# Optimization experiments

Hardware: AMD Instinct MI355X
Metric: run time of the kernel (lower is better)

The kernel has to match this reference:

```python
import jax, jax.numpy as jnp
import numpy as np

N = 16384       # nodes (hits in one event)
IN_DIM = 9      # input features per hit
HID = 128       # hidden_dim
PROP = 64       # propagate_dimensions; 2*PROP == HID so all gravnet layers share shapes
SPACE = 4       # learned space dimensions
K = 40          # neighbors (includes self, matching torch_cluster.knn)
L = 4           # num_gravnet_layers
OUT_DIM = 4


def _lin(key, fan_in, fan_out):
    # torch nn.Linear default init: U(-1/sqrt(fan_in), 1/sqrt(fan_in))
    k1, k2 = jax.random.split(key)
    lim = 1.0 / np.sqrt(fan_in)
    W = jax.random.uniform(k1, (fan_in, fan_out), minval=-lim, maxval=lim, dtype=jnp.float32)
    b = jax.random.uniform(k2, (fan_out,), minval=-lim, maxval=lim, dtype=jnp.float32)
    return W, b


def _stack_lin(key, fan_in, fan_out, n):
    Ws, bs = [], []
    for i in range(n):
        W, b = _lin(jax.random.fold_in(key, i), fan_in, fan_out)
        Ws.append(W); bs.append(b)
    return jnp.stack(Ws), jnp.stack(bs)


def setup_inputs() -> dict:
    key = jax.random.key(0)
    ks = jax.random.split(key, 16)
    inp = {}
    inp['x'] = jax.random.normal(ks[0], (N, IN_DIM), dtype=jnp.float32)
    inp['fc1_W'], inp['fc1_b'] = _lin(ks[1], IN_DIM, HID)
    inp['fc2_W'], inp['fc2_b'] = _lin(ks[2], HID, HID)
    # GravNetConv params (in_channels = HID = 2*PROP for every layer)
    inp['gs_W'], inp['gs_b'] = _stack_lin(ks[3], HID, SPACE, L)          # lin_s
    inp['gh_W'], inp['gh_b'] = _stack_lin(ks[4], HID, PROP, L)           # lin_h
    inp['go_W'], inp['go_b'] = _stack_lin(ks[5], HID + 2 * PROP, 2 * PROP, L)  # lin_out
    # dense_after_gravnet: Linear(2P->HID), Linear(HID->HID), Linear(HID->2P)
    inp['d1_W'], inp['d1_b'] = _stack_lin(ks[6], 2 * PROP, HID, L)
    inp['d2_W'], inp['d2_b'] = _stack_lin(ks[7], HID, HID, L)
    inp['d3_W'], inp['d3_b'] = _stack_lin(ks[8], HID, 2 * PROP, L)
    inp['fc3_W'], inp['fc3_b'] = _lin(ks[9], 2 * PROP, HID)
    inp['fc4_W'], inp['fc4_b'] = _lin(ks[10], HID, OUT_DIM)
    return inp


def _gravnet_layer(x, sW, sb, hW, hb, oW, ob):
    # PyG GravNetConv: s = lin_s(x), h = lin_h(x); kNN in s-space (self included);
    # edge weight exp(-10*d^2); message h_j*w; aggr = [mean, max]; out = lin_out([x, aggr]).
    s = x @ sW + sb                               # [N, SPACE]
    h = x @ hW + hb                               # [N, PROP]
    s2 = jnp.sum(s * s, axis=1)
    d2 = s2[:, None] + s2[None, :] - 2.0 * (s @ s.T)   # [N, N] squared distances
    neg_d2, idx = jax.lax.top_k(-d2, K)           # k nearest (self is its own nearest)
    w = jnp.exp(10.0 * jnp.minimum(neg_d2, 0.0))  # exp(-10*d2), clamped d2 >= 0
    msg = h[idx] * w[..., None]                   # [N, K, PROP] gather + weight
    agg = jnp.concatenate([msg.mean(axis=1), msg.max(axis=1)], axis=-1)  # [N, 2P]
    return jnp.concatenate([x, agg], axis=-1) @ oW + ob


def reference(x, fc1_W, fc1_b, fc2_W, fc2_b, gs_W, gs_b, gh_W, gh_b, go_W, go_b,
              d1_W, d1_b, d2_W, d2_b, d3_W, d3_b, fc3_W, fc3_b, fc4_W, fc4_b):
    relu = jax.nn.relu
    x = relu(x @ fc1_W + fc1_b)
    x = relu(x @ fc2_W + fc2_b)
    for i in range(L):  # small fixed layer count
        x = _gravnet_layer(x, gs_W[i], gs_b[i], gh_W[i], gh_b[i], go_W[i], go_b[i])
        x = relu(x @ d1_W[i] + d1_b[i])
        x = relu(x @ d2_W[i] + d2_b[i])
        x = relu(x @ d3_W[i] + d3_b[i])
    x = relu(x @ fc3_W + fc3_b)
    return x @ fc4_W + fc4_b
```

## Files before the change

kernel.cpp:

```cpp
#include <hip/hip_runtime.h>
#include <math.h>

#define NPTS     16384
#define KNN_K    40
#define KNN_CAPW 320

typedef unsigned short u16;
typedef __attribute__((ext_vector_type(8))) short bf16x8;
typedef __attribute__((ext_vector_type(4))) float f32x4;

static __device__ __forceinline__ float bf2f(unsigned short h) {
  return __uint_as_float(((unsigned)h) << 16);
}
static __device__ __forceinline__ unsigned short f2bf(float f) {
  unsigned u = __float_as_uint(f);
  unsigned r = (u + 0x7fffu + ((u >> 16) & 1u)) >> 16;
  return (unsigned short)r;
}
static __device__ __forceinline__ float ldf(const float* p) { return *p; }
static __device__ __forceinline__ float ldf(const unsigned short* p) { return bf2f(*p); }

static __device__ __forceinline__ float rfl(float x) {
  return __uint_as_float(__builtin_amdgcn_readfirstlane(__float_as_uint(x)));
}
static __device__ __forceinline__ unsigned mbcnt64(unsigned long long m) {
  return __builtin_amdgcn_mbcnt_hi((unsigned)(m >> 32),
                                   __builtin_amdgcn_mbcnt_lo((unsigned)m, 0u));
}

static __device__ __forceinline__ unsigned encf(float f) {
  unsigned b = __float_as_uint(f);
  return (b & 0x80000000u) ? ~b : (b | 0x80000000u);
}
static __device__ __forceinline__ float decf(unsigned e) {
  unsigned b = (e & 0x80000000u) ? (e ^ 0x80000000u) : ~e;
  return __uint_as_float(b);
}

#define WSPLIT_ELEMS 393216

__global__ __launch_bounds__(256, 8) void wsplit_k(
    const float* __restrict__ fc2W, const float* __restrict__ ghW,
    const float* __restrict__ goW,  const float* __restrict__ d1W,
    const float* __restrict__ d2W,  const float* __restrict__ d3W,
    const float* __restrict__ fc3W, u16* __restrict__ out)
{
  int e = blockIdx.x * 256 + threadIdx.x;
  const float* W; int base, M, K;
  if (e < 16384)       { W = fc2W; base = 0;      M = 128; K = 128; }
  else if (e < 49152)  { W = ghW;  base = 16384;  M = 64;  K = 128; }
  else if (e < 180224) { W = goW;  base = 49152;  M = 128; K = 256; }
  else if (e < 245760) { W = d1W;  base = 180224; M = 128; K = 128; }
  else if (e < 311296) { W = d2W;  base = 245760; M = 128; K = 128; }
  else if (e < 376832) { W = d3W;  base = 311296; M = 128; K = 128; }
  else                 { W = fc3W; base = 376832; M = 128; K = 128; }
  int li = e - base;
  float wv = W[li];
  u16 hi = f2bf(wv);
  u16 lo = f2bf(wv - bf2f(hi));
  int row = li / M;
  int n   = li % M;
  int l   = row / K;
  int kl  = row % K;
  int p   = n >> 6, c = n & 63;
  int kb  = kl >> 5, kk = kl & 31;
  u16* ob = out + 2 * base + l * (2 * K * M) + p * (K * 128) + kb * 4096;
  ob[c * 32 + kk] = hi;
  ob[2048 + c * 32 + kk] = lo;
}

template<bool RELU>
__global__ __launch_bounds__(256, 2) void gemm_mfma_k(
    const u16* __restrict__ A1, int lda1,
    const u16* __restrict__ A2, int lda2, int K1,
    const u16* __restrict__ Wsp, int pstride, const float* __restrict__ bias,
    u16* __restrict__ C, int ldc, int K)
{
  constexpr int MCOLS = 64;
  constexpr int AST = 40;
  __shared__ u16 lds[64 * AST + 2 * MCOLS * AST];
  u16* As = lds;
  u16* Wh = lds + 64 * AST;
  u16* Wl = Wh + MCOLS * AST;

  const int tid = threadIdx.x;
  const int lane = tid & 63;
  const int w = tid >> 6;
  const int panel = blockIdx.x >> 8;
  const int row0 = (blockIdx.x & 255) * 64;
  Wsp += (size_t)panel * pstride;
  bias += panel * 64;
  C += panel * 64;

  f32x4 acc[4];
  #pragma unroll
  for (int rt = 0; rt < 4; ++rt)
    acc[rt] = (f32x4){0.f, 0.f, 0.f, 0.f};

  const int rbase = lane & 15;
  const int koff = (lane >> 4) * 8;

  for (int k0 = 0, kb = 0; k0 < K; k0 += 32, ++kb) {
    __syncthreads();
    {
      int r = tid >> 2, seg = tid & 3;
      int kk = k0 + seg * 8;
      const u16* src = (kk < K1) ? &A1[(size_t)(row0 + r) * lda1 + kk]
                                 : &A2[(size_t)(row0 + r) * lda2 + (kk - K1)];
      *(uint4*)&As[r * AST + seg * 8] = *(const uint4*)src;
    }
    {
      const u16* wsb = Wsp + (size_t)kb * 4096;
      #pragma unroll
      for (int l = tid; l < 2 * MCOLS * 4; l += 256) {
        int r = l >> 2, seg = l & 3;
        *(uint4*)&Wh[r * AST + seg * 8] = *(const uint4*)&wsb[r * 32 + seg * 8];
      }
    }
    __syncthreads();

    bf16x8 a[4];
    #pragma unroll
    for (int rt = 0; rt < 4; ++rt)
      a[rt] = *(const bf16x8*)&As[(rt * 16 + rbase) * AST + koff];
    {
      int col = w * 16 + rbase;
      bf16x8 bh = *(const bf16x8*)&Wh[col * AST + koff];
      bf16x8 bl = *(const bf16x8*)&Wl[col * AST + koff];
      #pragma unroll
      for (int rt = 0; rt < 4; ++rt) {
        acc[rt] = __builtin_amdgcn_mfma_f32_16x16x32_bf16(a[rt], bh, acc[rt], 0, 0, 0);
        acc[rt] = __builtin_amdgcn_mfma_f32_16x16x32_bf16(a[rt], bl, acc[rt], 0, 0, 0);
      }
    }
  }

  __syncthreads();
  constexpr int CST = MCOLS + 8;
  u16* Ct = lds;
  const int rq = (lane >> 4) * 4;
  {
    int col = w * 16 + rbase;
    float bv = bias[col];
    #pragma unroll
    for (int rt = 0; rt < 4; ++rt) {
      #pragma unroll
      for (int q = 0; q < 4; ++q) {
        float v = acc[rt][q] + bv;
        if (RELU) v = fmaxf(v, 0.f);
        Ct[(rt * 16 + rq + q) * CST + col] = f2bf(v);
      }
    }
  }
  __syncthreads();
  constexpr int SEGS = MCOLS / 8;
  for (int l = tid; l < 64 * SEGS; l += 256) {
    int r = l / SEGS, sg = l % SEGS;
    *(uint4*)&C[(size_t)(row0 + r) * ldc + sg * 8] = *(const uint4*)&Ct[r * CST + sg * 8];
  }
}

template<int MCOLS, bool RELU>
__global__ __launch_bounds__(256, 2) void gemm_mfma_f32_k(
    const u16* __restrict__ A1, int lda1,
    const u16* __restrict__ A2, int lda2, int K1,
    const float* __restrict__ W, const float* __restrict__ bias,
    u16* __restrict__ C, int ldc, int K)
{
  constexpr int CT = MCOLS / 64;
  constexpr int AST = 40;
  __shared__ u16 lds[64 * AST + 2 * MCOLS * AST];
  u16* As = lds;
  u16* Wh = lds + 64 * AST;
  u16* Wl = Wh + MCOLS * AST;

  const int tid = threadIdx.x;
  const int lane = tid & 63;
  const int w = tid >> 6;
  const int row0 = blockIdx.x * 64;

  f32x4 acc[4][CT];
  #pragma unroll
  for (int rt = 0; rt < 4; ++rt)
    #pragma unroll
    for (int ct = 0; ct < CT; ++ct)
      acc[rt][ct] = (f32x4){0.f, 0.f, 0.f, 0.f};

  const int rbase = lane & 15;
  const int koff = (lane >> 4) * 8;

  for (int k0 = 0; k0 < K; k0 += 32) {
    __syncthreads();
    {
      int r = tid >> 2, seg = tid & 3;
      int kk = k0 + seg * 8;
      const u16* src = (kk < K1) ? &A1[(size_t)(row0 + r) * lda1 + kk]
                                 : &A2[(size_t)(row0 + r) * lda2 + (kk - K1)];
      *(uint4*)&As[r * AST + seg * 8] = *(const uint4*)src;
    }
    for (int l = tid; l < 32 * MCOLS; l += 256) {
      int n = l & (MCOLS - 1), kk = l / MCOLS;
      float wv = W[(size_t)(k0 + kk) * MCOLS + n];
      u16 h = f2bf(wv);
      Wh[n * AST + kk] = h;
      Wl[n * AST + kk] = f2bf(wv - bf2f(h));
    }
    __syncthreads();

    bf16x8 a[4];
    #pragma unroll
    for (int rt = 0; rt < 4; ++rt)
      a[rt] = *(const bf16x8*)&As[(rt * 16 + rbase) * AST + koff];
    #pragma unroll
    for (int ct = 0; ct < CT; ++ct) {
      int col = (w * CT + ct) * 16 + rbase;
      bf16x8 bh = *(const bf16x8*)&Wh[col * AST + koff];
      bf16x8 bl = *(const bf16x8*)&Wl[col * AST + koff];
      #pragma unroll
      for (int rt = 0; rt < 4; ++rt) {
        acc[rt][ct] = __builtin_amdgcn_mfma_f32_16x16x32_bf16(a[rt], bh, acc[rt][ct], 0, 0, 0);
        acc[rt][ct] = __builtin_amdgcn_mfma_f32_16x16x32_bf16(a[rt], bl, acc[rt][ct], 0, 0, 0);
      }
    }
  }

  __syncthreads();
  constexpr int CST = MCOLS + 8;
  u16* Ct = lds;
  const int rq = (lane >> 4) * 4;
  #pragma unroll
  for (int ct = 0; ct < CT; ++ct) {
    int col = (w * CT + ct) * 16 + rbase;
    float bv = bias[col];
    #pragma unroll
    for (int rt = 0; rt < 4; ++rt) {
      #pragma unroll
      for (int q = 0; q < 4; ++q) {
        float v = acc[rt][ct][q] + bv;
        if (RELU) v = fmaxf(v, 0.f);
        Ct[(rt * 16 + rq + q) * CST + col] = f2bf(v);
      }
    }
  }
  __syncthreads();
  constexpr int SEGS = MCOLS / 8;
  for (int l = tid; l < 64 * SEGS; l += 256) {
    int r = l / SEGS, sg = l % SEGS;
    *(uint4*)&C[(size_t)(row0 + r) * ldc + sg * 8] = *(const uint4*)&Ct[r * CST + sg * 8];
  }
}

template<int MCOLS, bool RELU, typename TIN, typename TOUT>
__global__ __launch_bounds__(256, 4) void gemm_k(
    const TIN* __restrict__ A1, int lda1,
    const TIN* __restrict__ A2, int lda2, int K1,
    const float* __restrict__ W, const float* __restrict__ bias,
    TOUT* __restrict__ C, int ldc, int K)
{
  constexpr int TCS = MCOLS / 8;
  constexpr int RPT = (64 * TCS) / 256;
  __shared__ float Asl[64][33];
  __shared__ float Ws[32][MCOLS];
  const int tid = threadIdx.x;
  const int row0 = blockIdx.x * 64;
  const int tc = tid % TCS, tr = tid / TCS;

  float acc[RPT][8];
  #pragma unroll
  for (int p = 0; p < RPT; ++p)
    #pragma unroll
    for (int q = 0; q < 8; ++q) acc[p][q] = 0.f;

  for (int k0 = 0; k0 < K; k0 += 32) {
    __syncthreads();
    for (int l = tid; l < 64 * 32; l += 256) {
      int r = l >> 5, c = l & 31, k = k0 + c;
      float v = 0.f;
      if (k < K) v = (k < K1) ? ldf(&A1[(size_t)(row0 + r) * lda1 + k])
                              : ldf(&A2[(size_t)(row0 + r) * lda2 + (k - K1)]);
      Asl[r][c] = v;
    }
    for (int l = tid; l < 32 * MCOLS; l += 256) {
      int kr = l / MCOLS, c = l % MCOLS, k = k0 + kr;
      Ws[kr][c] = (k < K) ? W[(size_t)k * MCOLS + c] : 0.f;
    }
    __syncthreads();
    #pragma unroll
    for (int kk = 0; kk < 32; ++kk) {
      float a[RPT];
      #pragma unroll
      for (int p = 0; p < RPT; ++p) a[p] = Asl[tr * RPT + p][kk];
      const float4 w0 = *(const float4*)&Ws[kk][tc * 8];
      const float4 w1 = *(const float4*)&Ws[kk][tc * 8 + 4];
      #pragma unroll
      for (int p = 0; p < RPT; ++p) {
        acc[p][0] = fmaf(a[p], w0.x, acc[p][0]);
        acc[p][1] = fmaf(a[p], w0.y, acc[p][1]);
        acc[p][2] = fmaf(a[p], w0.z, acc[p][2]);
        acc[p][3] = fmaf(a[p], w0.w, acc[p][3]);
        acc[p][4] = fmaf(a[p], w1.x, acc[p][4]);
        acc[p][5] = fmaf(a[p], w1.y, acc[p][5]);
        acc[p][6] = fmaf(a[p], w1.z, acc[p][6]);
        acc[p][7] = fmaf(a[p], w1.w, acc[p][7]);
      }
    }
  }

  const float4 b0 = *(const float4*)&bias[tc * 8];
  const float4 b1 = *(const float4*)&bias[tc * 8 + 4];
  #pragma unroll
  for (int p = 0; p < RPT; ++p) {
    int r = row0 + tr * RPT + p;
    float o[8];
    o[0] = acc[p][0] + b0.x; o[1] = acc[p][1] + b0.y;
    o[2] = acc[p][2] + b0.z; o[3] = acc[p][3] + b0.w;
    o[4] = acc[p][4] + b1.x; o[5] = acc[p][5] + b1.y;
    o[6] = acc[p][6] + b1.z; o[7] = acc[p][7] + b1.w;
    if (RELU) {
      #pragma unroll
      for (int q = 0; q < 8; ++q) o[q] = fmaxf(o[q], 0.f);
    }
    if constexpr (sizeof(TOUT) == 2) {
      unsigned p0 = (unsigned)f2bf(o[0]) | ((unsigned)f2bf(o[1]) << 16);
      unsigned p1 = (unsigned)f2bf(o[2]) | ((unsigned)f2bf(o[3]) << 16);
      unsigned p2 = (unsigned)f2bf(o[4]) | ((unsigned)f2bf(o[5]) << 16);
      unsigned p3 = (unsigned)f2bf(o[6]) | ((unsigned)f2bf(o[7]) << 16);
      uint4 pk = make_uint4(p0, p1, p2, p3);
      *(uint4*)&C[(size_t)r * ldc + tc * 8] = pk;
    } else {
      float4 o0, o1;
      o0.x = o[0]; o0.y = o[1]; o0.z = o[2]; o0.w = o[3];
      o1.x = o[4]; o1.y = o[5]; o1.z = o[6]; o1.w = o[7];
      *(float4*)&C[(size_t)r * ldc + tc * 8] = o0;
      *(float4*)&C[(size_t)r * ldc + tc * 8 + 4] = o1;
    }
  }
}

template<bool RELU, bool MM, typename TOUT>
__global__ __launch_bounds__(256, 4) void gemm4_k(
    const u16* __restrict__ A, int lda,
    const float* __restrict__ W, const float* __restrict__ bias,
    TOUT* __restrict__ C, int K, unsigned* mm)
{
  __shared__ float Wsl[128 * 4];
  __shared__ float bl[4];
  const int tid = threadIdx.x;
  for (int l = tid; l < K * 4; l += 256) Wsl[l] = W[l];
  if (tid < 4) bl[tid] = bias[tid];
  __syncthreads();
  const int row = blockIdx.x * 256 + tid;
  const u16* ap = A + (size_t)row * lda;
  float a0 = bl[0], a1 = bl[1], a2 = bl[2], a3 = bl[3];
  for (int k8 = 0; k8 < K; k8 += 8) {
    uint4 pk = *(const uint4*)&ap[k8];
    unsigned uu[4] = {pk.x, pk.y, pk.z, pk.w};
    #pragma unroll
    for (int q = 0; q < 4; ++q) {
      float flo = __uint_as_float(uu[q] << 16);
      float fhi = __uint_as_float(uu[q] & 0xFFFF0000u);
      const float* wr0 = &Wsl[(k8 + 2 * q) * 4];
      a0 = fmaf(flo, wr0[0], a0); a1 = fmaf(flo, wr0[1], a1);
      a2 = fmaf(flo, wr0[2], a2); a3 = fmaf(flo, wr0[3], a3);
      a0 = fmaf(fhi, wr0[4], a0); a1 = fmaf(fhi, wr0[5], a1);
      a2 = fmaf(fhi, wr0[6], a2); a3 = fmaf(fhi, wr0[7], a3);
    }
  }
  if (RELU) {
    a0 = fmaxf(a0, 0.f); a1 = fmaxf(a1, 0.f);
    a2 = fmaxf(a2, 0.f); a3 = fmaxf(a3, 0.f);
  }
  if constexpr (sizeof(TOUT) == 2) {
    C[(size_t)row * 4 + 0] = (TOUT)f2bf(a0);
    C[(size_t)row * 4 + 1] = (TOUT)f2bf(a1);
    C[(size_t)row * 4 + 2] = (TOUT)f2bf(a2);
    C[(size_t)row * 4 + 3] = (TOUT)f2bf(a3);
  } else {
    float4 o; o.x = a0; o.y = a1; o.z = a2; o.w = a3;
    *(float4*)&C[(size_t)row * 4] = o;
  }
  if constexpr (MM) {
    float mn0 = a0, mx0 = a0, mn1 = a1, mx1 = a1;
    float mn2 = a2, mx2 = a2, mn3 = a3, mx3 = a3;
    #pragma unroll
    for (int o = 32; o >= 1; o >>= 1) {
      mn0 = fminf(mn0, __shfl_xor(mn0, o, 64)); mx0 = fmaxf(mx0, __shfl_xor(mx0, o, 64));
      mn1 = fminf(mn1, __shfl_xor(mn1, o, 64)); mx1 = fmaxf(mx1, __shfl_xor(mx1, o, 64));
      mn2 = fminf(mn2, __shfl_xor(mn2, o, 64)); mx2 = fmaxf(mx2, __shfl_xor(mx2, o, 64));
      mn3 = fminf(mn3, __shfl_xor(mn3, o, 64)); mx3 = fmaxf(mx3, __shfl_xor(mx3, o, 64));
    }
    if ((tid & 63) == 0) {
      atomicMin(&mm[0], encf(mn0)); atomicMax(&mm[4], encf(mx0));
      atomicMin(&mm[1], encf(mn1)); atomicMax(&mm[5], encf(mx1));
      atomicMin(&mm[2], encf(mn2)); atomicMax(&mm[6], encf(mx2));
      atomicMin(&mm[3], encf(mn3)); atomicMax(&mm[7], encf(mx3));
    }
  }
}

__global__ void init_mm_k(unsigned* mm) {
  int t = threadIdx.x;
  if (t < 4) { mm[t] = 0xFFFFFFFFu; mm[4 + t] = 0u; }
}

static __device__ __forceinline__ float dimsel(float4 p, int d) {
  return (d == 0) ? p.x : (d == 1) ? p.y : (d == 2) ? p.z : p.w;
}

__global__ __launch_bounds__(1024, 1) void histpref_k(
    const float* __restrict__ S, unsigned* __restrict__ mm,
    unsigned* __restrict__ binoff)
{
  __shared__ unsigned hist[256];
  __shared__ unsigned wsum[4];
  const int tid = threadIdx.x;
  float mn[4], rg[4];
  #pragma unroll
  for (int d = 0; d < 4; ++d) {
    mn[d] = decf(mm[d]);
    rg[d] = decf(mm[4 + d]) - mn[d];
  }
  int a = 0;
  #pragma unroll
  for (int d = 1; d < 4; ++d) if (rg[d] > rg[a]) a = d;
  int b = (a == 0) ? 1 : 0;
  #pragma unroll
  for (int d = 0; d < 4; ++d) if (d != a && rg[d] > rg[b]) b = d;
  float inva = (rg[a] > 0.f) ? (16.f / rg[a]) * 0.999999f : 0.f;
  float invb = (rg[b] > 0.f) ? (16.f / rg[b]) * 0.999999f : 0.f;
  if (tid == 0) {
    mm[8] = (unsigned)a; mm[9] = (unsigned)b;
    mm[10] = __float_as_uint(mn[a]); mm[11] = __float_as_uint(inva);
    mm[12] = __float_as_uint(mn[b]); mm[13] = __float_as_uint(invb);
  }
  if (tid < 256) hist[tid] = 0u;
  __syncthreads();
  for (int i = tid; i < NPTS; i += 1024) {
    float4 p = *(const float4*)&S[(size_t)i * 4];
    int ba = min(15, max(0, (int)((dimsel(p, a) - mn[a]) * inva)));
    int bb = min(15, max(0, (int)((dimsel(p, b) - mn[b]) * invb)));
    atomicAdd(&hist[ba * 16 + bb], 1u);
  }
  __syncthreads();
  unsigned v = 0, x = 0;
  if (tid < 256) {
    int lane = tid & 63;
    v = hist[tid]; x = v;
    #pragma unroll
    for (int o = 1; o < 64; o <<= 1) {
      unsigned t = (unsigned)__shfl_up((int)x, o, 64);
      if (lane >= o) x += t;
    }
    if (lane == 63) wsum[tid >> 6] = x;
  }
  __syncthreads();
  if (tid < 256) {
    unsigned off = 0;
    for (int k = 0; k < (tid >> 6); ++k) off += wsum[k];
    binoff[tid] = off + x - v;
  }
}

__global__ __launch_bounds__(256, 4) void scatter_k(
    const float* __restrict__ S, const unsigned* __restrict__ mm,
    unsigned* __restrict__ binoff,
    float4* __restrict__ SX4, float* __restrict__ SS2, u16* __restrict__ SIDXs)
{
  int a = (int)mm[8], b = (int)mm[9];
  float alo = __uint_as_float(mm[10]), inva = __uint_as_float(mm[11]);
  float blo = __uint_as_float(mm[12]), invb = __uint_as_float(mm[13]);
  int i = blockIdx.x * 256 + threadIdx.x;
  float4 p = *(const float4*)&S[(size_t)i * 4];
  int ba = min(15, max(0, (int)((dimsel(p, a) - alo) * inva)));
  int bb = min(15, max(0, (int)((dimsel(p, b) - blo) * invb)));
  unsigned pos = atomicAdd(&binoff[ba * 16 + bb], 1u);
  SX4[pos] = p;
  SS2[pos] = fmaf(p.x, p.x, fmaf(p.y, p.y, fmaf(p.z, p.z, p.w * p.w)));
  SIDXs[pos] = (u16)i;
}

__global__ __launch_bounds__(512, 4) void gaabb_k(const float4* __restrict__ SX4,
                                                  float* __restrict__ gaabb) {
  int w = threadIdx.x >> 6, lane = threadIdx.x & 63;
  int g = blockIdx.x * 8 + w;
  float4 p = SX4[g * 64 + lane];
  float mnx = p.x, mny = p.y, mnz = p.z, mnw = p.w;
  float mxx = p.x, mxy = p.y, mxz = p.z, mxw = p.w;
  #pragma unroll
  for (int o = 32; o >= 1; o >>= 1) {
    mnx = fminf(mnx, __shfl_xor(mnx, o, 64)); mxx = fmaxf(mxx, __shfl_xor(mxx, o, 64));
    mny = fminf(mny, __shfl_xor(mny, o, 64)); mxy = fmaxf(mxy, __shfl_xor(mxy, o, 64));
    mnz = fminf(mnz, __shfl_xor(mnz, o, 64)); mxz = fmaxf(mxz, __shfl_xor(mxz, o, 64));
    mnw = fminf(mnw, __shfl_xor(mnw, o, 64)); mxw = fmaxf(mxw, __shfl_xor(mxw, o, 64));
  }
  if (lane == 0) {
    float4* gp = (float4*)&gaabb[g * 8];
    gp[0] = make_float4(mnx, mny, mnz, mnw);
    gp[1] = make_float4(mxx, mxy, mxz, mxw);
  }
}

struct CompactRes { int cnt; unsigned thr; };

static __device__ __forceinline__ CompactRes compact_buf(unsigned* bufR, int cnt, int lane) {
  int n = min(cnt, KNN_CAPW);
  int lo = -1, hi = 0x7FFFFFFF, chi = n;
  for (int it = 0; it < 32; ++it) {
    if (chi <= 96) break;
    int mid = lo + ((hi - lo) >> 1);
    int lc = 0;
    for (int base = 0; base < n; base += 64) {
      int i = base + lane;
      bool c = (i < n) && (bufR[i] <= (unsigned)mid);
      lc += (int)__popcll(__ballot(c));
    }
    if (lc >= 40) { hi = mid; chi = lc; } else lo = mid;
  }
  unsigned thr = (unsigned)hi;
  int out = 0;
  for (int base = 0; base < n; base += 64) {
    int i = base + lane;
    unsigned key = (i < n) ? bufR[i] : 0xFFFFFFFFu;
    bool keep = (i < n) && (key <= thr);
    unsigned long long mk = __ballot(keep);
    unsigned pre = mbcnt64(mk);
    if (keep) bufR[out + (int)pre] = key;
    out += (int)__popcll(mk);
  }
  CompactRes r; r.cnt = out; r.thr = thr;
  return r;
}

__global__ __launch_bounds__(256, 4) void knn_k(
    const float4* __restrict__ SX4, const float* __restrict__ SS2,
    const u16* __restrict__ SIDXs, const float* __restrict__ gaabb,
    u16* __restrict__ idx_out, u16* __restrict__ w_out)
{
  __shared__ unsigned buf[4 * 4 * KNN_CAPW];
  __shared__ unsigned scr[4 * 128];
  __shared__ int cnts[16];
  __shared__ unsigned thrend[16];
  __shared__ unsigned short glist[4 * 64];
  __shared__ unsigned long long mws[4];
  __shared__ unsigned thrsh[4];

  const int tid = threadIdx.x;
  const int lane = tid & 63;
  const int w = tid >> 6;
  const int sp0 = blockIdx.x * 4;

  float cx[4], cy[4], cz[4], cw[4], s2r[4], thrF[4];
  int orow[4], cnt[4];
  #pragma unroll
  for (int r = 0; r < 4; ++r) {
    float4 sr = SX4[sp0 + r];
    cx[r] = rfl(-2.f * sr.x); cy[r] = rfl(-2.f * sr.y);
    cz[r] = rfl(-2.f * sr.z); cw[r] = rfl(-2.f * sr.w);
    s2r[r] = rfl(fmaf(sr.x, sr.x, fmaf(sr.y, sr.y, fmaf(sr.z, sr.z, sr.w * sr.w))));
    orow[r] = SIDXs[sp0 + r];
    cnt[r] = 0;
  }
  unsigned* bufw = &buf[w * 4 * KNN_CAPW];
  unsigned* mph = buf;

  {
    int gs = sp0 >> 6;
    int g0 = min(max(gs - 7, 0), 240);
    float m1[4], m2[4];
    #pragma unroll
    for (int r = 0; r < 4; ++r) { m1[r] = 3.0e38f; m2[r] = 3.0e38f; }
    #pragma unroll
    for (int gi = 0; gi < 4; ++gi) {
      int j = (g0 + w * 4 + gi) * 64 + lane;
      float4 p = SX4[j];
      float q = SS2[j];
      #pragma unroll
      for (int r = 0; r < 4; ++r) {
        float d = fmaf(cx[r], p.x, fmaf(cy[r], p.y, fmaf(cz[r], p.z,
                  fmaf(cw[r], p.w, q + s2r[r]))));
        d = fmaxf(d, 0.f);
        bool lt1 = d < m1[r];
        float nm2 = lt1 ? m1[r] : fminf(m2[r], d);
        m1[r] = fminf(m1[r], d);
        m2[r] = nm2;
      }
    }
    #pragma unroll
    for (int r = 0; r < 4; ++r) {
      mph[(r * 8 + w * 2 + 0) * 64 + lane] = __float_as_uint(m1[r]);
      mph[(r * 8 + w * 2 + 1) * 64 + lane] = __float_as_uint(m2[r]);
    }
  }
  __syncthreads();

  {
    unsigned m1 = 0xFFFFFFFFu, m2 = 0xFFFFFFFFu;
    #pragma unroll
    for (int s = 0; s < 8; ++s) {
      unsigned v = mph[(w * 8 + s) * 64 + lane];
      bool lt = v < m1;
      unsigned nm2 = lt ? m1 : min(m2, v);
      m1 = min(m1, v);
      m2 = nm2;
    }
    unsigned e0 = m1, e1 = m2;
    #pragma unroll
    for (int k = 2; k <= 128; k <<= 1) {
      #pragma unroll
      for (int jj = k >> 1; jj >= 1; jj >>= 1) {
        bool up = (((lane * 2) & k) == 0);
        if (jj == 1) {
          unsigned a = min(e0, e1), b = max(e0, e1);
          e0 = up ? a : b; e1 = up ? b : a;
        } else {
          int lj = jj >> 1;
          bool lower = ((lane & lj) == 0);
          bool tm = (up == lower);
          unsigned o0 = (unsigned)__shfl_xor((int)e0, lj, 64);
          e0 = tm ? min(e0, o0) : max(e0, o0);
          unsigned o1 = (unsigned)__shfl_xor((int)e1, lj, 64);
          e1 = tm ? min(e1, o1) : max(e1, o1);
        }
      }
    }
    unsigned v40 = (unsigned)__shfl((int)e1, 19, 64);
    if (lane == 0) thrsh[w] = v40;
  }
  __syncthreads();
  #pragma unroll
  for (int r = 0; r < 4; ++r) thrF[r] = __uint_as_float(thrsh[r]);

  {
    int g = w * 64 + lane;
    float4 mn = *(const float4*)&gaabb[g * 8];
    float4 mx = *(const float4*)&gaabb[g * 8 + 4];
    bool want = false;
    #pragma unroll
    for (int r = 0; r < 4; ++r) {
      float px = -0.5f * cx[r], py = -0.5f * cy[r];
      float pz = -0.5f * cz[r], pw = -0.5f * cw[r];
      float dx = fmaxf(fmaxf(mn.x - px, px - mx.x), 0.f);
      float dy = fmaxf(fmaxf(mn.y - py, py - mx.y), 0.f);
      float dz = fmaxf(fmaxf(mn.z - pz, pz - mx.z), 0.f);
      float dw = fmaxf(fmaxf(mn.w - pw, pw - mx.w), 0.f);
      float md = fmaf(dx, dx, fmaf(dy, dy, fmaf(dz, dz, dw * dw)));
      want |= (md <= thrF[r]);
    }
    unsigned long long bal = __ballot(want);
    if (lane == 0) mws[w] = bal;
  }
  __syncthreads();

  int ng = 0;
  {
    int ordbase = 0;
    #pragma unroll
    for (int pgi = 0; pgi < 4; ++pgi) {
      unsigned long long m = mws[pgi];
      bool want = (m >> lane) & 1ull;
      int ord = ordbase + (int)mbcnt64(m);
      if (want && ((ord & 3) == w))
        glist[w * 64 + (ord >> 2)] = (unsigned short)(pgi * 64 + lane);
      ordbase += (int)__popcll(m);
    }
    ng = (ordbase + 3 - w) >> 2;
  }

  if (ng > 0) {
    int j = (int)glist[w * 64] * 64 + lane;
    float4 p = SX4[j];
    float q = SS2[j];
    unsigned sv = (unsigned)j;
    for (int i = 0; i < ng; ++i) {
      float4 pn = p; float qn = q; unsigned svn = sv;
      if (i + 1 < ng) {
        int j2 = (int)glist[w * 64 + i + 1] * 64 + lane;
        pn = SX4[j2]; qn = SS2[j2]; svn = (unsigned)j2;
      }
      #pragma unroll
      for (int r = 0; r < 4; ++r) {
        float d = fmaf(cx[r], p.x, fmaf(cy[r], p.y, fmaf(cz[r], p.z,
                  fmaf(cw[r], p.w, q + s2r[r]))));
        bool k = d <= thrF[r];
        unsigned long long mk = __ballot(k);
        if (mk) {
          int pos = cnt[r] + (int)mbcnt64(mk);
          if (k) bufw[r * KNN_CAPW + pos] =
              (__float_as_uint(fmaxf(d, 0.f)) & 0xFFFFC000u) | sv;
          cnt[r] += (int)__popcll(mk);
          if (cnt[r] >= KNN_CAPW - 64) {
            CompactRes cr = compact_buf(&bufw[r * KNN_CAPW], cnt[r], lane);
            cnt[r] = cr.cnt;
            thrF[r] = __uint_as_float((cr.thr & 0xFFFFC000u) | 0x3FFFu);
          }
        }
      }
      p = pn; q = qn; sv = svn;
    }
  }

  if (lane == 0) {
    #pragma unroll
    for (int r = 0; r < 4; ++r) {
      cnts[w * 4 + r] = cnt[r];
      thrend[w * 4 + r] = (__float_as_uint(thrF[r]) & 0xFFFFC000u) | 0x3FFFu;
    }
  }
  __syncthreads();

  {
    const int rr = w;
    const unsigned* seg[4];
    int c[4], off[5];
    off[0] = 0;
    #pragma unroll
    for (int s = 0; s < 4; ++s) {
      seg[s] = &buf[(s * 4 + rr) * KNN_CAPW];
      c[s] = cnts[s * 4 + rr];
      off[s + 1] = off[s] + c[s];
    }
    int mt = off[4];
    unsigned* S = &scr[rr * 128];

    if (mt > 128) {
      unsigned hi0 = min(min(thrend[0 * 4 + rr], thrend[1 * 4 + rr]),
                         min(thrend[2 * 4 + rr], thrend[3 * 4 + rr]));
      int lc = 0;
      #pragma unroll
      for (int s = 0; s < 4; ++s)
        for (int base = 0; base < c[s]; base += 64) {
          int i = base + lane;
          bool cc = (i < c[s]) && (seg[s][i] <= hi0);
          lc += (int)__popcll(__ballot(cc));
        }
      unsigned thrm = hi0;
      if (lc > 128) {
        int lo = -1, hi = (int)hi0, chi = lc;
        for (int it = 0; it < 32; ++it) {
          if (chi <= 96) break;
          int mid = lo + ((hi - lo) >> 1);
          int lc2 = 0;
          #pragma unroll
          for (int s = 0; s < 4; ++s)
            for (int base = 0; base < c[s]; base += 64) {
              int i = base + lane;
              bool cc = (i < c[s]) && (seg[s][i] <= (unsigned)mid);
              lc2 += (int)__popcll(__ballot(cc));
            }
          if (lc2 >= 40) { hi = mid; chi = lc2; } else lo = mid;
        }
        thrm = (unsigned)hi;
      }
      int out = 0;
      #pragma unroll
      for (int s = 0; s < 4; ++s)
        for (int base = 0; base < c[s]; base += 64) {
          int i = base + lane;
          unsigned key = (i < c[s]) ? seg[s][i] : 0xFFFFFFFFu;
          bool keep = (i < c[s]) && (key <= thrm);
          unsigned long long mk = __ballot(keep);
          int pos = out + (int)mbcnt64(mk);
          if (keep && pos < 128) S[pos] = key;
          out += (int)__popcll(mk);
        }
      mt = min(out, 128);
    } else {
      #pragma unroll
      for (int s = 0; s < 4; ++s)
        for (int base = 0; base < c[s]; base += 64) {
          int i = base + lane;
          if (i < c[s]) S[off[s] + i] = seg[s][i];
        }
    }

    const float fx = cx[rr], fy = cy[rr], fz = cz[rr], fw = cw[rr];
    const float s2i = s2r[rr];
    const int row = orow[rr];

    unsigned long long e0 = ~0ull, e1 = ~0ull;
    {
      int sl0 = lane * 2, sl1 = lane * 2 + 1;
      if (sl0 < mt) {
        unsigned key = S[sl0];
        unsigned sj = key & 0x3FFFu;
        float4 p = SX4[sj];
        float qj = fmaf(p.x, p.x, fmaf(p.y, p.y, fmaf(p.z, p.z, p.w * p.w)));
        float d = fmaf(fx, p.x, fmaf(fy, p.y, fmaf(fz, p.z, fmaf(fw, p.w, qj + s2i))));
        unsigned oi = (unsigned)SIDXs[sj];
        e0 = (((unsigned long long)__float_as_uint(fmaxf(d, 0.f))) << 32) | oi;
      }
      if (sl1 < mt) {
        unsigned key = S[sl1];
        unsigned sj = key & 0x3FFFu;
        float4 p = SX4[sj];
        float qj = fmaf(p.x, p.x, fmaf(p.y, p.y, fmaf(p.z, p.z, p.w * p.w)));
        float d = fmaf(fx, p.x, fmaf(fy, p.y, fmaf(fz, p.z, fmaf(fw, p.w, qj + s2i))));
        unsigned oi = (unsigned)SIDXs[sj];
        e1 = (((unsigned long long)__float_as_uint(fmaxf(d, 0.f))) << 32) | oi;
      }
    }

    #pragma unroll
    for (int k = 2; k <= 128; k <<= 1) {
      #pragma unroll
      for (int jj = k >> 1; jj >= 1; jj >>= 1) {
        bool up = (((lane * 2) & k) == 0);
        if (jj == 1) {
          unsigned long long a = (e0 < e1) ? e0 : e1;
          unsigned long long b = (e0 < e1) ? e1 : e0;
          e0 = up ? a : b; e1 = up ? b : a;
        } else {
          int lj = jj >> 1;
          bool lower = ((lane & lj) == 0);
          bool tm = (up == lower);
          unsigned long long o0 = __shfl_xor(e0, lj, 64);
          e0 = tm ? ((e0 < o0) ? e0 : o0) : ((e0 > o0) ? e0 : o0);
          unsigned long long o1 = __shfl_xor(e1, lj, 64);
          e1 = tm ? ((e1 < o1) ? e1 : o1) : ((e1 > o1) ? e1 : o1);
        }
      }
    }

    const int ob = row * KNN_K;
    if (lane < 20) {
      int v0 = lane * 2;
      idx_out[ob + v0] = (unsigned short)(e0 & 0xFFFFu);
      w_out[ob + v0] = f2bf(__expf(-10.f * __uint_as_float((unsigned)(e0 >> 32))));
      int v1 = v0 + 1;
      idx_out[ob + v1] = (unsigned short)(e1 & 0xFFFFu);
      w_out[ob + v1] = f2bf(__expf(-10.f * __uint_as_float((unsigned)(e1 >> 32))));
    }
  }
}

__global__ __launch_bounds__(256, 4) void agg_k(
    const unsigned short* __restrict__ h, const unsigned short* __restrict__ idxb,
    const unsigned short* __restrict__ wb, unsigned short* __restrict__ Aout)
{
  const int row = blockIdx.x * 4 + (threadIdx.x >> 6);
  const int lane = threadIdx.x & 63;
  const int base = row * KNN_K;
  float mean = 0.f, mx = -INFINITY;
  #pragma unroll 4
  for (int k = 0; k < KNN_K; ++k) {
    int j = idxb[base + k];
    float wv = bf2f(wb[base + k]);
    float m = bf2f(h[(size_t)j * 64 + lane]) * wv;
    mean += m;
    mx = fmaxf(mx, m);
  }
  Aout[(size_t)row * 128 + lane] = f2bf(mean * (1.f / 40.f));
  Aout[(size_t)row * 128 + 64 + lane] = f2bf(mx);
}

extern "C" void kernel_launch(void* const* d_in, const int* in_sizes, int n_in,
                              void* d_out, int out_size, void* d_ws, size_t ws_size,
                              hipStream_t stream)
{
  const float* x    = (const float*)d_in[0];
  const float* fc1W = (const float*)d_in[1];  const float* fc1b = (const float*)d_in[2];
  const float* fc2W = (const float*)d_in[3];  const float* fc2b = (const float*)d_in[4];
  const float* gsW  = (const float*)d_in[5];  const float* gsb  = (const float*)d_in[6];
  const float* ghW  = (const float*)d_in[7];  const float* ghb  = (const float*)d_in[8];
  const float* goW  = (const float*)d_in[9];  const float* gob  = (const float*)d_in[10];
  const float* d1W  = (const float*)d_in[11]; const float* d1b  = (const float*)d_in[12];
  const float* d2W  = (const float*)d_in[13]; const float* d2b  = (const float*)d_in[14];
  const float* d3W  = (const float*)d_in[15]; const float* d3b  = (const float*)d_in[16];
  const float* fc3W = (const float*)d_in[17]; const float* fc3b = (const float*)d_in[18];
  const float* fc4W = (const float*)d_in[19]; const float* fc4b = (const float*)d_in[20];
  float* out = (float*)d_out;

  const size_t N = NPTS;
  u16* X    = (u16*)d_ws;
  u16* Abuf = X + N * 128;
  u16* T    = Abuf + N * 128;
  u16* IDX  = T + N * 128;
  u16* WNB  = IDX + N * 40;
  float4* SX4g = (float4*)(WNB + N * 40);
  float*  SS2g = (float*)(SX4g + N);
  u16*    SIDXg = (u16*)(SS2g + N);
  unsigned* binoff = (unsigned*)(SIDXg + N);
  unsigned* mm     = binoff + 256;
  float* gaabbg    = (float*)(mm + 16);
  float* S = (float*)Abuf;
  u16* H = T;

  u16* WSPL = (u16*)(gaabbg + 256 * 8);
  size_t needed = (size_t)((char*)(WSPL + 2ull * WSPLIT_ELEMS) - (char*)d_ws);
  const bool PRE = ws_size >= needed;

  const size_t OF_FC2 = 0,      OF_GH = 32768, OF_GO = 98304;
  const size_t OF_D1 = 360448,  OF_D2 = 491520, OF_D3 = 622592, OF_FC3 = 753664;
  const int PS_128 = 16384;
  const int PS_256 = 32768;
  const size_t LS_GH = 16384, LS_GO = 65536, LS_D = 32768;

  if (PRE) {
    wsplit_k<<<WSPLIT_ELEMS / 256, 256, 0, stream>>>(
        fc2W, ghW, goW, d1W, d2W, d3W, fc3W, WSPL);
  }

  gemm_k<128, true, float, u16><<<NPTS / 64, 256, 0, stream>>>(
      x, 9, x, 9, 9, fc1W, fc1b, T, 128, 9);
  if (PRE)
    gemm_mfma_k<true><<<512, 256, 0, stream>>>(
        T, 128, T, 128, 128, WSPL + OF_FC2, PS_128, fc2b, X, 128, 128);
  else
    gemm_mfma_f32_k<128, true><<<NPTS / 64, 256, 0, stream>>>(
        T, 128, T, 128, 128, fc2W, fc2b, X, 128, 128);

  for (int l = 0; l < 4; ++l) {
    init_mm_k<<<1, 64, 0, stream>>>(mm);
    gemm4_k<false, true, float><<<NPTS / 256, 256, 0, stream>>>(
        X, 128, gsW + l * 128 * 4, gsb + l * 4, S, 128, mm);
    if (PRE)
      gemm_mfma_k<false><<<256, 256, 0, stream>>>(
          X, 128, X, 128, 128, WSPL + OF_GH + l * LS_GH, PS_128, ghb + l * 64, H, 64, 128);
    else
      gemm_mfma_f32_k<64, false><<<NPTS / 64, 256, 0, stream>>>(
          X, 128, X, 128, 128, ghW + l * 128 * 64, ghb + l * 64, H, 64, 128);
    histpref_k<<<1, 1024, 0, stream>>>(S, mm, binoff);
    scatter_k<<<NPTS / 256, 256, 0, stream>>>(S, mm, binoff, SX4g, SS2g, SIDXg);
    gaabb_k<<<32, 512, 0, stream>>>(SX4g, gaabbg);
    knn_k<<<NPTS / 4, 256, 0, stream>>>(SX4g, SS2g, SIDXg, gaabbg, IDX, WNB);
    agg_k<<<NPTS / 4, 256, 0, stream>>>(H, IDX, WNB, Abuf);
    if (PRE) {
      gemm_mfma_k<false><<<512, 256, 0, stream>>>(
          X, 128, Abuf, 128, 128, WSPL + OF_GO + l * LS_GO, PS_256, gob + l * 128, T, 128, 256);
      gemm_mfma_k<true><<<512, 256, 0, stream>>>(
          T, 128, T, 128, 128, WSPL + OF_D1 + l * LS_D, PS_128, d1b + l * 128, Abuf, 128, 128);
      gemm_mfma_k<true><<<512, 256, 0, stream>>>(
          Abuf, 128, Abuf, 128, 128, WSPL + OF_D2 + l * LS_D, PS_128, d2b + l * 128, T, 128, 128);
      gemm_mfma_k<true><<<512, 256, 0, stream>>>(
          T, 128, T, 128, 128, WSPL + OF_D3 + l * LS_D, PS_128, d3b + l * 128, X, 128, 128);
    } else {
      gemm_mfma_f32_k<128, false><<<NPTS / 64, 256, 0, stream>>>(
          X, 128, Abuf, 128, 128, goW + l * 256 * 128, gob + l * 128, T, 128, 256);
      gemm_mfma_f32_k<128, true><<<NPTS / 64, 256, 0, stream>>>(
          T, 128, T, 128, 128, d1W + l * 128 * 128, d1b + l * 128, Abuf, 128, 128);
      gemm_mfma_f32_k<128, true><<<NPTS / 64, 256, 0, stream>>>(
          Abuf, 128, Abuf, 128, 128, d2W + l * 128 * 128, d2b + l * 128, T, 128, 128);
      gemm_mfma_f32_k<128, true><<<NPTS / 64, 256, 0, stream>>>(
          T, 128, T, 128, 128, d3W + l * 128 * 128, d3b + l * 128, X, 128, 128);
    }
  }

  if (PRE)
    gemm_mfma_k<true><<<512, 256, 0, stream>>>(
        X, 128, X, 128, 128, WSPL + OF_FC3, PS_128, fc3b, T, 128, 128);
  else
    gemm_mfma_f32_k<128, true><<<NPTS / 64, 256, 0, stream>>>(
        X, 128, X, 128, 128, fc3W, fc3b, T, 128, 128);
  gemm4_k<false, false, float><<<NPTS / 256, 256, 0, stream>>>(
      T, 128, fc4W, fc4b, out, 128, mm);
}
```

Before: 1.016 ms.

## Parallelize kNN binning histogram across blocks and raise kNN occupancy

Replaces the single-block, 1024-thread histogram-plus-prefix kernel with a grid-wide histogram kernel that uses global atomics, followed by a small one-block prefix kernel. The prefix kernel also resets the histogram and min/max state, so the per-layer init launch moves out of the loop and runs once. Separately, the kNN candidate buffer capacity per wave drops from 320 to 256 and the kNN kernel's launch bounds ask for 8 blocks per CU instead of 4, to raise occupancy. The smaller candidate buffer could overflow more often on dense neighbourhoods, and global atomics on 256 bins may contend.

```diff
diff --git a/kernel.cpp b/kernel.cpp
--- a/kernel.cpp
+++ b/kernel.cpp
@@ -3,7 +3,7 @@
 
 #define NPTS     16384
 #define KNN_K    40
-#define KNN_CAPW 320
+#define KNN_CAPW 256
 
 typedef unsigned short u16;
 typedef __attribute__((ext_vector_type(8))) short bf16x8;
@@ -398,67 +398,77 @@
   }
 }
 
-__global__ void init_mm_k(unsigned* mm) {
+__global__ void init_mm_k(unsigned* mm, unsigned* ghist) {
   int t = threadIdx.x;
   if (t < 4) { mm[t] = 0xFFFFFFFFu; mm[4 + t] = 0u; }
+  ghist[t] = 0u;
 }
 
 static __device__ __forceinline__ float dimsel(float4 p, int d) {
   return (d == 0) ? p.x : (d == 1) ? p.y : (d == 2) ? p.z : p.w;
 }
 
-__global__ __launch_bounds__(1024, 1) void histpref_k(
-    const float* __restrict__ S, unsigned* __restrict__ mm,
-    unsigned* __restrict__ binoff)
-{
-  __shared__ unsigned hist[256];
-  __shared__ unsigned wsum[4];
-  const int tid = threadIdx.x;
+static __device__ __forceinline__ void derive_bins(
+    const unsigned* mm, int& a, int& b, float& mna, float& inva,
+    float& mnb, float& invb)
+{
   float mn[4], rg[4];
   #pragma unroll
   for (int d = 0; d < 4; ++d) {
     mn[d] = decf(mm[d]);
     rg[d] = decf(mm[4 + d]) - mn[d];
   }
-  int a = 0;
+  a = 0;
   #pragma unroll
   for (int d = 1; d < 4; ++d) if (rg[d] > rg[a]) a = d;
-  int b = (a == 0) ? 1 : 0;
+  b = (a == 0) ? 1 : 0;
   #pragma unroll
   for (int d = 0; d < 4; ++d) if (d != a && rg[d] > rg[b]) b = d;
-  float inva = (rg[a] > 0.f) ? (16.f / rg[a]) * 0.999999f : 0.f;
-  float invb = (rg[b] > 0.f) ? (16.f / rg[b]) * 0.999999f : 0.f;
+  mna = mn[a]; mnb = mn[b];
+  inva = (rg[a] > 0.f) ? (16.f / rg[a]) * 0.999999f : 0.f;
+  invb = (rg[b] > 0.f) ? (16.f / rg[b]) * 0.999999f : 0.f;
+}
+
+__global__ __launch_bounds__(256, 8) void hist_k(
+    const float* __restrict__ S, const unsigned* __restrict__ mm,
+    unsigned* __restrict__ ghist)
+{
+  int a, b; float mna, inva, mnb, invb;
+  derive_bins(mm, a, b, mna, inva, mnb, invb);
+  int i = blockIdx.x * 256 + threadIdx.x;
+  float4 p = *(const float4*)&S[(size_t)i * 4];
+  int ba = min(15, max(0, (int)((dimsel(p, a) - mna) * inva)));
+  int bb = min(15, max(0, (int)((dimsel(p, b) - mnb) * invb)));
+  atomicAdd(&ghist[ba * 16 + bb], 1u);
+}
+
+__global__ __launch_bounds__(256, 4) void pref_k(
+    unsigned* __restrict__ mm, unsigned* __restrict__ ghist,
+    unsigned* __restrict__ binoff)
+{
+  __shared__ unsigned wsum[4];
+  const int tid = threadIdx.x;
+  int a, b; float mna, inva, mnb, invb;
+  derive_bins(mm, a, b, mna, inva, mnb, invb);
   if (tid == 0) {
     mm[8] = (unsigned)a; mm[9] = (unsigned)b;
-    mm[10] = __float_as_uint(mn[a]); mm[11] = __float_as_uint(inva);
-    mm[12] = __float_as_uint(mn[b]); mm[13] = __float_as_uint(invb);
-  }
-  if (tid < 256) hist[tid] = 0u;
+    mm[10] = __float_as_uint(mna); mm[11] = __float_as_uint(inva);
+    mm[12] = __float_as_uint(mnb); mm[13] = __float_as_uint(invb);
+  }
+  int lane = tid & 63;
+  unsigned v = ghist[tid], x = v;
+  #pragma unroll
+  for (int o = 1; o < 64; o <<= 1) {
+    unsigned t = (unsigned)__shfl_up((int)x, o, 64);
+    if (lane >= o) x += t;
+  }
+  if (lane == 63) wsum[tid >> 6] = x;
   __syncthreads();
-  for (int i = tid; i < NPTS; i += 1024) {
-    float4 p = *(const float4*)&S[(size_t)i * 4];
-    int ba = min(15, max(0, (int)((dimsel(p, a) - mn[a]) * inva)));
-    int bb = min(15, max(0, (int)((dimsel(p, b) - mn[b]) * invb)));
-    atomicAdd(&hist[ba * 16 + bb], 1u);
-  }
-  __syncthreads();
-  unsigned v = 0, x = 0;
-  if (tid < 256) {
-    int lane = tid & 63;
-    v = hist[tid]; x = v;
-    #pragma unroll
-    for (int o = 1; o < 64; o <<= 1) {
-      unsigned t = (unsigned)__shfl_up((int)x, o, 64);
-      if (lane >= o) x += t;
-    }
-    if (lane == 63) wsum[tid >> 6] = x;
-  }
-  __syncthreads();
-  if (tid < 256) {
-    unsigned off = 0;
-    for (int k = 0; k < (tid >> 6); ++k) off += wsum[k];
-    binoff[tid] = off + x - v;
-  }
+  unsigned off = 0;
+  for (int k = 0; k < (tid >> 6); ++k) off += wsum[k];
+  binoff[tid] = off + x - v;
+  ghist[tid] = 0u;
+  if (tid < 8) mm[tid] = (tid < 4) ? 0xFFFFFFFFu : 0u;
 }
 
 __global__ __launch_bounds__(256, 4) void scatter_k(
@@ -531,7 +541,7 @@
   return r;
 }
 
-__global__ __launch_bounds__(256, 4) void knn_k(
+__global__ __launch_bounds__(256, 8) void knn_k(
     const float4* __restrict__ SX4, const float* __restrict__ SS2,
     const u16* __restrict__ SIDXs, const float* __restrict__ gaabb,
     u16* __restrict__ idx_out, u16* __restrict__ w_out)
@@ -882,10 +892,11 @@
   unsigned* binoff = (unsigned*)(SIDXg + N);
   unsigned* mm     = binoff + 256;
   float* gaabbg    = (float*)(mm + 16);
+  unsigned* ghist  = (unsigned*)(gaabbg + 256 * 8);
   float* S = (float*)Abuf;
   u16* H = T;
 
-  u16* WSPL = (u16*)(gaabbg + 256 * 8);
+  u16* WSPL = (u16*)(ghist + 256);
   size_t needed = (size_t)((char*)(WSPL + 2ull * WSPLIT_ELEMS) - (char*)d_ws);
   const bool PRE = ws_size >= needed;
 
@@ -899,6 +910,8 @@
     wsplit_k<<<WSPLIT_ELEMS / 256, 256, 0, stream>>>(
         fc2W, ghW, goW, d1W, d2W, d3W, fc3W, WSPL);
   }
+
+  init_mm_k<<<1, 256, 0, stream>>>(mm, ghist);
 
   gemm_k<128, true, float, u16><<<NPTS / 64, 256, 0, stream>>>(
       x, 9, x, 9, 9, fc1W, fc1b, T, 128, 9);
@@ -910,7 +923,6 @@
         T, 128, T, 128, 128, fc2W, fc2b, X, 128, 128);
 
   for (int l = 0; l < 4; ++l) {
-    init_mm_k<<<1, 64, 0, stream>>>(mm);
     gemm4_k<false, true, float><<<NPTS / 256, 256, 0, stream>>>(
         X, 128, gsW + l * 128 * 4, gsb + l * 4, S, 128, mm);
     if (PRE)
@@ -919,7 +931,8 @@
     else
       gemm_mfma_f32_k<64, false><<<NPTS / 64, 256, 0, stream>>>(
           X, 128, X, 128, 128, ghW + l * 128 * 64, ghb + l * 64, H, 64, 128);
-    histpref_k<<<1, 1024, 0, stream>>>(S, mm, binoff);
+    hist_k<<<NPTS / 256, 256, 0, stream>>>(S, mm, ghist);
+    pref_k<<<1, 256, 0, stream>>>(mm, ghist, binoff);
     scatter_k<<<NPTS / 256, 256, 0, stream>>>(S, mm, binoff, SX4g, SS2g, SIDXg);
     gaabb_k<<<32, 512, 0, stream>>>(SX4g, gaabbg);
     knn_k<<<NPTS / 4, 256, 0, stream>>>(SX4g, SS2g, SIDXg, gaabbg, IDX, WNB);
```

Result: slower. 1.136 ms (+11.8%).
